# Kernel optimization log

Hardware: AMD Instinct MI355X
Metric: run time of the kernel (lower is better)

## Reference

```python
import jax, jax.numpy as jnp
import numpy as np

B, N, NNZ = 512, 512, 8192
ENTITY, EMB, HID = 30000, 64, 100
PAD_ID = ENTITY - 1


def setup_inputs() -> dict:
    key = jax.random.key(0)
    ks = jax.random.split(key, 8)
    hyperneigh = jax.random.randint(ks[0], (B, N), 0, PAD_ID, dtype=jnp.int64)
    adj_rows = jax.random.randint(ks[1], (B, NNZ), 0, N, dtype=jnp.int32)
    adj_cols = jax.random.randint(ks[2], (B, NNZ), 0, N, dtype=jnp.int32)
    adj_vals = jax.random.uniform(ks[3], (B, NNZ), dtype=jnp.float32)
    emb_table = jax.random.normal(ks[4], (ENTITY, EMB), dtype=jnp.float32)
    emb_table = emb_table.at[PAD_ID].set(0.0)  # padding_idx row is zero
    stdv1 = 1.0 / np.sqrt(HID)
    W1 = jax.random.uniform(ks[5], (EMB, HID), minval=-stdv1, maxval=stdv1, dtype=jnp.float32)
    b1 = jax.random.uniform(ks[6], (HID,), minval=-stdv1, maxval=stdv1, dtype=jnp.float32)
    k7, k8 = jax.random.split(ks[7])
    W2 = jax.random.uniform(k7, (HID, HID), minval=-stdv1, maxval=stdv1, dtype=jnp.float32)
    b2 = jax.random.uniform(k8, (HID,), minval=-stdv1, maxval=stdv1, dtype=jnp.float32)
    return dict(hyperneigh=hyperneigh, adj_rows=adj_rows, adj_cols=adj_cols,
                adj_vals=adj_vals, emb_table=emb_table, W1=W1, b1=b1, W2=W2, b2=b2)


def _spmm(rows, cols, vals, X):
    # sparse [N,N] @ X[N,H] via gather + segment_sum (COO, fixed nnz)
    msgs = vals[:, None] * X[cols]  # [nnz, H]
    return jax.ops.segment_sum(msgs, rows, num_segments=N)

_batched_spmm = jax.vmap(_spmm, in_axes=(0, 0, 0, 0))


def reference(hyperneigh, adj_rows, adj_cols, adj_vals, emb_table, W1, b1, W2, b2):
    # embedding lookup: [B, N, EMB]
    x = emb_table[hyperneigh]
    # HGNN_conv layer 1: support = X @ W; out = A @ support + bias
    support = jnp.einsum('bne,eh->bnh', x, W1)
    x = _batched_spmm(adj_rows, adj_cols, adj_vals, support) + b1
    # HGNN_conv layer 2
    support = jnp.einsum('bnh,hk->bnk', x, W2)
    x = _batched_spmm(adj_rows, adj_cols, adj_vals, support) + b2
    return x  # [B, N, HID]
```

## Files before the change

### kernel.cpp

```cpp
#include <hip/hip_runtime.h>

#define BB   512
#define NN   512
#define NNZ  8192
#define EMB  64
#define HID  100
#define EXCAP 128

#define OFF_RC      0
#define OFF_VPK     16777216
#define OFF_SSTART  25165824
#define OFF_SUPT    26216448
#define OFF_W1T     84936704
#define OFF_W2T     84951040

typedef __attribute__((ext_vector_type(8))) short short8;
typedef __attribute__((ext_vector_type(4))) float floatx4;

__device__ __forceinline__ unsigned short f2bf(float f) {
    unsigned u = __float_as_uint(f);
    unsigned r = (u + 0x7fffu + ((u >> 16) & 1u)) >> 16;
    return (unsigned short)r;
}

__device__ __forceinline__ float bf2f(unsigned short b) {
    return __uint_as_float((unsigned)b << 16);
}

__device__ __forceinline__ short8 pack8(float4 a, float4 b) {
    short8 s;
    s[0] = (short)f2bf(a.x); s[1] = (short)f2bf(a.y);
    s[2] = (short)f2bf(a.z); s[3] = (short)f2bf(a.w);
    s[4] = (short)f2bf(b.x); s[5] = (short)f2bf(b.y);
    s[6] = (short)f2bf(b.z); s[7] = (short)f2bf(b.w);
    return s;
}

__device__ __forceinline__ size_t supt_addr(int batch, int col, int k) {
    return (size_t)batch * 57344 + (size_t)(k >> 5) * 3584 + (size_t)col * 32 + (k & 31);
}

__device__ __forceinline__ int ad_addr(int rr, int c) {
    return (rr >> 4) * 8192 + (c >> 5) * 512 + ((c >> 3) & 3) * 128 + (rr & 15) * 8 + (c & 7);
}

__global__ __launch_bounds__(512) void k_bucket(
    const int* __restrict__ rows, const int* __restrict__ cols,
    const float* __restrict__ vals, int* __restrict__ rc,
    unsigned short* __restrict__ vpk, int* __restrict__ sstart,
    const float* __restrict__ W1, const float* __restrict__ W2,
    unsigned short* __restrict__ w1t, unsigned short* __restrict__ w2t)
{
    __shared__ int            rl[NNZ];
    __shared__ unsigned short vh[NNZ];
    __shared__ int            wcnt[8][8];
    __shared__ int            wbase[8][8];

    const int b   = blockIdx.x;
    const int tid = threadIdx.x;
    const int lane = tid & 63, wave = tid >> 6;

    {
        int pid = b + (tid << 9);
        if (pid < 7168) {
            int h = pid >> 6, k = pid & 63;
            w1t[pid] = f2bf((h < 100) ? W1[k * 100 + h] : 0.f);
        } else if (pid < 7168 + 14336) {
            int id2 = pid - 7168;
            int h = id2 >> 7, k = id2 & 127;
            w2t[id2] = f2bf((h < 100 && k < 100) ? W2[k * 100 + h] : 0.f);
        }
    }

    const int*   rb = rows + (size_t)b * NNZ;
    const int*   cb = cols + (size_t)b * NNZ;
    const float* vb = vals + (size_t)b * NNZ;

    int rr[16], cc[16];
    float vv[16];
    #pragma unroll
    for (int i = 0; i < 16; ++i) {
        int idx = tid + i * 512;
        rr[i] = rb[idx]; cc[i] = cb[idx]; vv[i] = vb[idx];
    }

    if (tid < 64) ((int*)wcnt)[tid] = 0;
    __syncthreads();

    #pragma unroll
    for (int i = 0; i < 16; ++i)
        atomicAdd(&wcnt[wave][rr[i] >> 6], 1);
    __syncthreads();

    if (tid == 0) {
        int acc = 0;
        #pragma unroll
        for (int s = 0; s < 8; ++s) {
            sstart[b * 9 + s] = acc;
            #pragma unroll
            for (int w = 0; w < 8; ++w) { wbase[w][s] = acc; acc += wcnt[w][s]; }
        }
        sstart[b * 9 + 8] = NNZ;
    }
    __syncthreads();
    if (tid < 64) ((int*)wcnt)[tid] = ((int*)wbase)[tid];
    __syncthreads();

    #pragma unroll
    for (int i = 0; i < 16; ++i) {
        int s = rr[i] >> 6;
        int pos = atomicAdd(&wcnt[wave][s], 1);
        rl[pos] = (rr[i] << 16) | cc[i];
        vh[pos] = f2bf(vv[i]);
    }
    __syncthreads();

    {
        int* orc = rc + (size_t)b * NNZ;
        #pragma unroll
        for (int i = 0; i < 16; ++i) {
            int idx = tid + i * 512;
            orc[idx] = rl[idx];
        }
        unsigned* ov = (unsigned*)(vpk + (size_t)b * NNZ);
        #pragma unroll
        for (int i = 0; i < 8; ++i) {
            int p = tid + i * 512;
            ov[p] = (unsigned)vh[2 * p] | ((unsigned)vh[2 * p + 1] << 16);
        }
    }
}

__global__ __launch_bounds__(256) void k_gemm1_mfma(
    const int* __restrict__ hyper, const float* __restrict__ emb,
    const unsigned short* __restrict__ w1t, unsigned short* __restrict__ supT)
{
    const int lane = threadIdx.x & 63, wave = threadIdx.x >> 6;
    const int l15 = lane & 15, g4 = lane >> 4;

    short8 bq[7][2];
    #pragma unroll
    for (int ct = 0; ct < 7; ++ct)
        #pragma unroll
        for (int kt = 0; kt < 2; ++kt)
            bq[ct][kt] = *(const short8*)(w1t + (ct * 16 + l15) * 64 + kt * 32 + g4 * 8);

    const int wsid = blockIdx.x * 4 + wave;
    #pragma unroll 2
    for (int i = 0; i < 4; ++i) {
        const int  rb   = wsid * 4 + i;
        const long base = (long)rb * 16;
        const int  rid  = hyper[base + l15];
        const float* ep = emb + (long)rid * EMB + g4 * 8;
        float4 f0 = *(const float4*)(ep);
        float4 f1 = *(const float4*)(ep + 4);
        float4 f2 = *(const float4*)(ep + 32);
        float4 f3 = *(const float4*)(ep + 36);
        short8 a0 = pack8(f0, f1);
        short8 a1 = pack8(f2, f3);

        floatx4 acc[7];
        #pragma unroll
        for (int ct = 0; ct < 7; ++ct) acc[ct] = (floatx4)0.f;
        #pragma unroll
        for (int ct = 0; ct < 7; ++ct) {
            acc[ct] = __builtin_amdgcn_mfma_f32_16x16x32_bf16(a0, bq[ct][0], acc[ct], 0, 0, 0);
            acc[ct] = __builtin_amdgcn_mfma_f32_16x16x32_bf16(a1, bq[ct][1], acc[ct], 0, 0, 0);
        }

        const int batch = rb >> 5;
        const int inrow = (rb & 31) * 16 + g4 * 4;
        #pragma unroll
        for (int ct = 0; ct < 7; ++ct) {
            int col = ct * 16 + l15;
            uint2 w;
            w.x = (unsigned)f2bf(acc[ct][0]) | ((unsigned)f2bf(acc[ct][1]) << 16);
            w.y = (unsigned)f2bf(acc[ct][2]) | ((unsigned)f2bf(acc[ct][3]) << 16);
            *(uint2*)(supT + supt_addr(batch, col, inrow)) = w;
        }
    }
}

__global__ __launch_bounds__(256) void k_gemm2_mfma(
    const unsigned short* __restrict__ h1, const unsigned short* __restrict__ w2t,
    unsigned short* __restrict__ supT)
{
    const int lane = threadIdx.x & 63, wave = threadIdx.x >> 6;
    const int l15 = lane & 15, g4 = lane >> 4;
    const int ct0 = (wave & 1) ? 4 : 0;

    short8 bq[4][4];
    #pragma unroll
    for (int ctl = 0; ctl < 4; ++ctl) {
        int ct = ct0 + ctl;
        if (ct < 7)
            #pragma unroll
            for (int kt = 0; kt < 4; ++kt)
                bq[ctl][kt] = *(const short8*)(w2t + (ct * 16 + l15) * 128 + kt * 32 + g4 * 8);
    }

    const int wp = blockIdx.x * 2 + (wave >> 1);
    #pragma unroll 2
    for (int i = 0; i < 8; ++i) {
        const int  rb   = wp * 8 + i;
        const long base = (long)rb * 16;
        const unsigned short* rp = h1 + (size_t)(base + l15) * 112;

        short8 a[4];
        #pragma unroll
        for (int kt = 0; kt < 4; ++kt) {
            int k0 = kt * 32 + g4 * 8;
            short8 av = (short8)(short)0;
            if (k0 < 112) av = *(const short8*)(rp + k0);
            a[kt] = av;
        }

        floatx4 acc[4];
        #pragma unroll
        for (int ctl = 0; ctl < 4; ++ctl) acc[ctl] = (floatx4)0.f;
        #pragma unroll
        for (int ctl = 0; ctl < 4; ++ctl) {
            if (ct0 + ctl < 7) {
                #pragma unroll
                for (int kt = 0; kt < 4; ++kt)
                    acc[ctl] = __builtin_amdgcn_mfma_f32_16x16x32_bf16(a[kt], bq[ctl][kt], acc[ctl], 0, 0, 0);
            }
        }

        const int batch = rb >> 5;
        const int inrow = (rb & 31) * 16 + g4 * 4;
        #pragma unroll
        for (int ctl = 0; ctl < 4; ++ctl) {
            if (ct0 + ctl < 7) {
                int col = (ct0 + ctl) * 16 + l15;
                uint2 w;
                w.x = (unsigned)f2bf(acc[ctl][0]) | ((unsigned)f2bf(acc[ctl][1]) << 16);
                w.y = (unsigned)f2bf(acc[ctl][2]) | ((unsigned)f2bf(acc[ctl][3]) << 16);
                *(uint2*)(supT + supt_addr(batch, col, inrow)) = w;
            }
        }
    }
}

template<bool FINAL>
__global__ __launch_bounds__(512, 4) void k_spmm_mfma(
    const int* __restrict__ sstart, const int* __restrict__ rc,
    const unsigned short* __restrict__ vpk, const unsigned short* __restrict__ supT,
    const float* __restrict__ bias, unsigned short* __restrict__ h1,
    float* __restrict__ out)
{
    __shared__ unsigned short Ad[64 * 512];
    __shared__ unsigned       bmap[64 * 16];
    __shared__ int            exc_rc[EXCAP];
    __shared__ unsigned short exc_v[EXCAP];
    __shared__ int            exn;

    const int tid    = threadIdx.x;
    const int xcd    = blockIdx.x & 7;
    const int local  = blockIdx.x >> 3;
    const int batch  = xcd * 64 + (local >> 3);
    const int stripe = local & 7;
    const int r0     = stripe * 64;

    const int lane = tid & 63, wave = tid >> 6;
    const int l15 = lane & 15, g4 = lane >> 4;
    const int ng  = wave & 3, kh = wave >> 2;
    const int nt0 = ng * 2;
    const bool two = (nt0 + 1) < 7;
    const int ktb = kh * 8;

    const int s0 = sstart[batch * 9 + stripe];
    const int e0 = sstart[batch * 9 + stripe + 1];
    const int*            rcb = rc + (size_t)batch * NNZ;
    const unsigned short* vvb = vpk + (size_t)batch * NNZ;
    int            pc[3];
    unsigned short pv[3];
    #pragma unroll
    for (int i = 0; i < 3; ++i) {
        int idx = s0 + tid + i * 512;
        bool ok = idx < e0;
        pc[i] = ok ? rcb[idx] : 0;
        pv[i] = ok ? vvb[idx] : 0;
    }

    const unsigned short* b0p = supT + (size_t)batch * 57344 + (size_t)ktb * 3584
                               + (nt0 * 16 + l15) * 32 + g4 * 8;
    const unsigned short* b1p = b0p + 512;
    short8 bfr[8];
    #pragma unroll
    for (int kt = 0; kt < 8; ++kt)
        bfr[kt] = *(const short8*)(b0p + (size_t)kt * 3584);

    {
        uint4* z = (uint4*)Ad;
        #pragma unroll
        for (int i = 0; i < 8; ++i) z[tid + i * 512] = make_uint4(0u, 0u, 0u, 0u);
        if (tid < 256) ((uint4*)bmap)[tid] = make_uint4(0u, 0u, 0u, 0u);
        if (tid == 0) exn = 0;
    }
    __syncthreads();

    #pragma unroll
    for (int i = 0; i < 3; ++i) {
        int idx = s0 + tid + i * 512;
        if (idx < e0) {
            int rr = ((pc[i] >> 16) & 0xffff) - r0;
            int c  = pc[i] & 0xffff;
            unsigned bit = 1u << (c & 31);
            unsigned old = atomicOr(&bmap[(rr << 4) + (c >> 5)], bit);
            if (old & bit) {
                int e = atomicAdd(&exn, 1);
                if (e < EXCAP) { exc_rc[e] = (rr << 9) | c; exc_v[e] = pv[i]; }
            } else {
                Ad[ad_addr(rr, c)] = pv[i];
            }
        }
    }
    for (int idx = s0 + 1536 + tid; idx < e0; idx += 512) {
        int p = rcb[idx];
        int rr = ((p >> 16) & 0xffff) - r0;
        int c  = p & 0xffff;
        unsigned bit = 1u << (c & 31);
        unsigned old = atomicOr(&bmap[(rr << 4) + (c >> 5)], bit);
        if (old & bit) {
            int e = atomicAdd(&exn, 1);
            if (e < EXCAP) { exc_rc[e] = (rr << 9) | c; exc_v[e] = vvb[idx]; }
        } else {
            Ad[ad_addr(rr, c)] = vvb[idx];
        }
    }
    __syncthreads();

    {
        int ne = exn < EXCAP ? exn : EXCAP;
        for (int t = tid; t < ne; t += 512) {
            int key = exc_rc[t];
            bool first = true;
            for (int j = 0; j < t; ++j)
                if (exc_rc[j] == key) { first = false; break; }
            if (first) {
                float add = bf2f(exc_v[t]);
                for (int j = t + 1; j < ne; ++j)
                    if (exc_rc[j] == key) add += bf2f(exc_v[j]);
                int rr = key >> 9, c = key & 511;
                int a = ad_addr(rr, c);
                Ad[a] = f2bf(bf2f(Ad[a]) + add);
            }
        }
    }
    __syncthreads();

    const unsigned short* ap = Ad + (size_t)ktb * 512 + lane * 8;

    floatx4 acc[2][4];
    #pragma unroll
    for (int n = 0; n < 2; ++n)
        #pragma unroll
        for (int m = 0; m < 4; ++m) acc[n][m] = (floatx4)0.f;

    #pragma unroll
    for (int kt = 0; kt < 8; ++kt) {
        short8 b1 = (short8)(short)0;
        if (two) b1 = *(const short8*)(b1p + (size_t)kt * 3584);
        #pragma unroll
        for (int m = 0; m < 4; ++m) {
            short8 a = *(const short8*)(ap + m * 8192 + kt * 512);
            acc[0][m] = __builtin_amdgcn_mfma_f32_16x16x32_bf16(a, bfr[kt], acc[0][m], 0, 0, 0);
            if (two)
                acc[1][m] = __builtin_amdgcn_mfma_f32_16x16x32_bf16(a, b1, acc[1][m], 0, 0, 0);
        }
    }
    __syncthreads();

    float* redu = (float*)Ad;
    if (kh == 1) {
        #pragma unroll
        for (int nn = 0; nn < 2; ++nn)
            #pragma unroll
            for (int m = 0; m < 4; ++m)
                #pragma unroll
                for (int q = 0; q < 4; ++q)
                    redu[ng * 2048 + ((nn * 4 + m) * 4 + q) * 64 + lane] = acc[nn][m][q];
    }
    __syncthreads();

    if (kh == 0) {
        #pragma unroll
        for (int nn = 0; nn < 2; ++nn)
            #pragma unroll
            for (int m = 0; m < 4; ++m)
                #pragma unroll
                for (int q = 0; q < 4; ++q)
                    acc[nn][m][q] += redu[ng * 2048 + ((nn * 4 + m) * 4 + q) * 64 + lane];

        if (FINAL) {
            float* st = (float*)((char*)Ad + 32768);
            #pragma unroll
            for (int nn = 0; nn < 2; ++nn) {
                int nt = nt0 + nn;
                if (nt >= 7) break;
                int col = nt * 16 + l15;
                float bi = (col < HID) ? bias[col] : 0.f;
                #pragma unroll
                for (int m = 0; m < 4; ++m) {
                    int row = m * 16 + g4 * 4;
                    #pragma unroll
                    for (int q = 0; q < 4; ++q)
                        st[(row + q) * 112 + col] = acc[nn][m][q] + bi;
                }
            }
        } else {
            unsigned short* st = (unsigned short*)((char*)Ad + 32768);
            #pragma unroll
            for (int nn = 0; nn < 2; ++nn) {
                int nt = nt0 + nn;
                if (nt >= 7) break;
                int col = nt * 16 + l15;
                float bi = (col < HID) ? bias[col] : 0.f;
                #pragma unroll
                for (int m = 0; m < 4; ++m) {
                    int row = m * 16 + g4 * 4;
                    #pragma unroll
                    for (int q = 0; q < 4; ++q)
                        st[(row + q) * 112 + col] = f2bf(acc[nn][m][q] + bi);
                }
            }
        }
    }
    __syncthreads();

    if (FINAL) {
        const float* st = (const float*)((char*)Ad + 32768);
        #pragma unroll
        for (int i = 0; i < 4; ++i) {
            int flat = tid + i * 512;
            if (flat < 1600) {
                int row = flat / 25, wi = flat - row * 25;
                float4 v = *(const float4*)(st + row * 112 + wi * 4);
                *(float4*)(out + ((size_t)batch * NN + r0 + row) * HID + wi * 4) = v;
            }
        }
    } else {
        const unsigned short* st = (const unsigned short*)((char*)Ad + 32768);
        #pragma unroll
        for (int i = 0; i < 2; ++i) {
            int flat = tid + i * 512;
            if (flat < 896) {
                int row = flat / 14, wi = flat - row * 14;
                uint4 v = *(const uint4*)(st + row * 112 + wi * 8);
                *(uint4*)(h1 + ((size_t)batch * NN + r0 + row) * 112 + wi * 8) = v;
            }
        }
    }
}

extern "C" void kernel_launch(void* const* d_in, const int* in_sizes, int n_in,
                              void* d_out, int out_size, void* d_ws, size_t ws_size,
                              hipStream_t stream)
{
    const int*   hyper = (const int*)  d_in[0];
    const int*   arows = (const int*)  d_in[1];
    const int*   acols = (const int*)  d_in[2];
    const float* avals = (const float*)d_in[3];
    const float* emb   = (const float*)d_in[4];
    const float* W1    = (const float*)d_in[5];
    const float* b1    = (const float*)d_in[6];
    const float* W2    = (const float*)d_in[7];
    const float* b2    = (const float*)d_in[8];

    float*          out = (float*)d_out;
    unsigned short* h1  = (unsigned short*)d_out;
    char*           ws  = (char*)d_ws;

    int*            rc     = (int*)           (ws + OFF_RC);
    unsigned short* vpk    = (unsigned short*)(ws + OFF_VPK);
    int*            sstart = (int*)           (ws + OFF_SSTART);
    unsigned short* supT   = (unsigned short*)(ws + OFF_SUPT);
    unsigned short* w1t    = (unsigned short*)(ws + OFF_W1T);
    unsigned short* w2t    = (unsigned short*)(ws + OFF_W2T);

    k_bucket<<<BB, 512, 0, stream>>>(arows, acols, avals, rc, vpk, sstart,
                                     W1, W2, w1t, w2t);

    k_gemm1_mfma<<<1024, 256, 0, stream>>>(hyper, emb, w1t, supT);
    k_spmm_mfma<false><<<BB * 8, 512, 0, stream>>>(sstart, rc, vpk, supT, b1, h1, out);
    k_gemm2_mfma<<<1024, 256, 0, stream>>>(h1, w2t, supT);
    k_spmm_mfma<true><<<BB * 8, 512, 0, stream>>>(sstart, rc, vpk, supT, b2, h1, out);
}
```

Before: 236.2 us.

## Detect duplicate COO entries once in bucket kernel instead of per spmm

Duplicate (row,col) detection moves from each spmm launch into the bucketing kernel. It uses a global bitmap (memset each call) and a per-batch exception list, with duplicates marked by a sentinel column. Each spmm then scatters non-duplicates into the dense tile without shared atomics and adds the exceptions from a preloaded list. The B-fragment loads also move into the MFMA loop with partial unroll, which lowers register use. The cost is a 16MB global memset plus global atomics in the bucket kernel, and every stripe block scans the whole batch's exception list.

```diff
diff --git a/kernel.cpp b/kernel.cpp
--- a/kernel.cpp
+++ b/kernel.cpp
@@ -5,7 +5,8 @@
 #define NNZ  8192
 #define EMB  64
 #define HID  100
-#define EXCAP 128
+#define EXCAPB 512
+#define DUPC 0x7FFF
 
 #define OFF_RC      0
 #define OFF_VPK     16777216
@@ -13,6 +14,10 @@
 #define OFF_SUPT    26216448
 #define OFF_W1T     84936704
 #define OFF_W2T     84951040
+#define OFF_BMAPG   84979712
+#define OFF_EXCNT   101756928
+#define OFF_EXK     101758976
+#define OFF_EXV     102807552
 
 typedef __attribute__((ext_vector_type(8))) short short8;
 typedef __attribute__((ext_vector_type(4))) float floatx4;
@@ -48,6 +53,8 @@
     const int* __restrict__ rows, const int* __restrict__ cols,
     const float* __restrict__ vals, int* __restrict__ rc,
     unsigned short* __restrict__ vpk, int* __restrict__ sstart,
+    unsigned* __restrict__ bmap_g, int* __restrict__ exc_cnt,
+    int* __restrict__ exc_k, float* __restrict__ exc_v,
     const float* __restrict__ W1, const float* __restrict__ W2,
     unsigned short* __restrict__ w1t, unsigned short* __restrict__ w2t)
 {
@@ -58,7 +65,7 @@
 
     const int b   = blockIdx.x;
     const int tid = threadIdx.x;
-    const int lane = tid & 63, wave = tid >> 6;
+    const int wave = tid >> 6;
 
     {
         int pid = b + (tid << 9);
@@ -84,6 +91,24 @@
         rr[i] = rb[idx]; cc[i] = cb[idx]; vv[i] = vb[idx];
     }
 
+    unsigned* bm = bmap_g + (size_t)b * 8192;
+    unsigned dupmask = 0;
+    #pragma unroll
+    for (int i = 0; i < 16; ++i) {
+        unsigned bit = 1u << (cc[i] & 31);
+        unsigned old = atomicOr(&bm[(rr[i] << 4) + (cc[i] >> 5)], bit);
+        if (old & bit) {
+            dupmask |= 1u << i;
+            int e = atomicAdd(&exc_cnt[b], 1);
+            if (e < EXCAPB) {
+                exc_k[b * EXCAPB + e] = (rr[i] << 9) | cc[i];
+                exc_v[b * EXCAPB + e] = vv[i];
+            } else {
+                dupmask &= ~(1u << i);
+            }
+        }
+    }
+
     if (tid < 64) ((int*)wcnt)[tid] = 0;
     __syncthreads();
 
@@ -110,8 +135,9 @@
     for (int i = 0; i < 16; ++i) {
         int s = rr[i] >> 6;
         int pos = atomicAdd(&wcnt[wave][s], 1);
-        rl[pos] = (rr[i] << 16) | cc[i];
-        vh[pos] = f2bf(vv[i]);
+        bool dup = (dupmask >> i) & 1;
+        rl[pos] = (rr[i] << 16) | (dup ? DUPC : cc[i]);
+        vh[pos] = dup ? 0 : f2bf(vv[i]);
     }
     __syncthreads();
 
@@ -246,14 +272,13 @@
 __global__ __launch_bounds__(512, 4) void k_spmm_mfma(
     const int* __restrict__ sstart, const int* __restrict__ rc,
     const unsigned short* __restrict__ vpk, const unsigned short* __restrict__ supT,
-    const float* __restrict__ bias, unsigned short* __restrict__ h1,
-    float* __restrict__ out)
+    const int* __restrict__ exc_cnt, const int* __restrict__ exc_k,
+    const float* __restrict__ exc_v, const float* __restrict__ bias,
+    unsigned short* __restrict__ h1, float* __restrict__ out)
 {
     __shared__ unsigned short Ad[64 * 512];
-    __shared__ unsigned       bmap[64 * 16];
-    __shared__ int            exc_rc[EXCAP];
-    __shared__ unsigned short exc_v[EXCAP];
-    __shared__ int            exn;
+    __shared__ int            lk[EXCAPB];
+    __shared__ float          lv[EXCAPB];
 
     const int tid    = threadIdx.x;
     const int xcd    = blockIdx.x & 7;
@@ -271,6 +296,7 @@
 
     const int s0 = sstart[batch * 9 + stripe];
     const int e0 = sstart[batch * 9 + stripe + 1];
+    const int ne = min(exc_cnt[batch], EXCAPB);
     const int*            rcb = rc + (size_t)batch * NNZ;
     const unsigned short* vvb = vpk + (size_t)batch * NNZ;
     int            pc[3];
@@ -282,21 +308,15 @@
         pc[i] = ok ? rcb[idx] : 0;
         pv[i] = ok ? vvb[idx] : 0;
     }
-
-    const unsigned short* b0p = supT + (size_t)batch * 57344 + (size_t)ktb * 3584
-                               + (nt0 * 16 + l15) * 32 + g4 * 8;
-    const unsigned short* b1p = b0p + 512;
-    short8 bfr[8];
-    #pragma unroll
-    for (int kt = 0; kt < 8; ++kt)
-        bfr[kt] = *(const short8*)(b0p + (size_t)kt * 3584);
+    if (tid < ne) {
+        lk[tid] = exc_k[batch * EXCAPB + tid];
+        lv[tid] = exc_v[batch * EXCAPB + tid];
+    }
 
     {
         uint4* z = (uint4*)Ad;
         #pragma unroll
         for (int i = 0; i < 8; ++i) z[tid + i * 512] = make_uint4(0u, 0u, 0u, 0u);
-        if (tid < 256) ((uint4*)bmap)[tid] = make_uint4(0u, 0u, 0u, 0u);
-        if (tid == 0) exn = 0;
     }
     __syncthreads();
 
@@ -306,51 +326,39 @@
         if (idx < e0) {
             int rr = ((pc[i] >> 16) & 0xffff) - r0;
             int c  = pc[i] & 0xffff;
-            unsigned bit = 1u << (c & 31);
-            unsigned old = atomicOr(&bmap[(rr << 4) + (c >> 5)], bit);
-            if (old & bit) {
-                int e = atomicAdd(&exn, 1);
-                if (e < EXCAP) { exc_rc[e] = (rr << 9) | c; exc_v[e] = pv[i]; }
-            } else {
-                Ad[ad_addr(rr, c)] = pv[i];
-            }
+            if (c < 512) Ad[ad_addr(rr, c)] = pv[i];
         }
     }
     for (int idx = s0 + 1536 + tid; idx < e0; idx += 512) {
         int p = rcb[idx];
         int rr = ((p >> 16) & 0xffff) - r0;
         int c  = p & 0xffff;
-        unsigned bit = 1u << (c & 31);
-        unsigned old = atomicOr(&bmap[(rr << 4) + (c >> 5)], bit);
-        if (old & bit) {
-            int e = atomicAdd(&exn, 1);
-            if (e < EXCAP) { exc_rc[e] = (rr << 9) | c; exc_v[e] = vvb[idx]; }
-        } else {
-            Ad[ad_addr(rr, c)] = vvb[idx];
-        }
-    }
-    __syncthreads();
-
-    {
-        int ne = exn < EXCAP ? exn : EXCAP;
-        for (int t = tid; t < ne; t += 512) {
-            int key = exc_rc[t];
-            bool first = true;
-            for (int j = 0; j < t; ++j)
-                if (exc_rc[j] == key) { first = false; break; }
-            if (first) {
-                float add = bf2f(exc_v[t]);
-                for (int j = t + 1; j < ne; ++j)
-                    if (exc_rc[j] == key) add += bf2f(exc_v[j]);
-                int rr = key >> 9, c = key & 511;
-                int a = ad_addr(rr, c);
-                Ad[a] = f2bf(bf2f(Ad[a]) + add);
-            }
-        }
-    }
-    __syncthreads();
-
-    const unsigned short* ap = Ad + (size_t)ktb * 512 + lane * 8;
+        if (c < 512) Ad[ad_addr(rr, c)] = vvb[idx];
+    }
+    __syncthreads();
+
+    for (int t = tid; t < ne; t += 512) {
+        int key = lk[t];
+        int r   = key >> 9;
+        if ((r >> 6) != stripe) continue;
+        bool first = true;
+        for (int j = 0; j < t; ++j)
+            if (lk[j] == key) { first = false; break; }
+        if (first) {
+            float add = lv[t];
+            for (int j = t + 1; j < ne; ++j)
+                if (lk[j] == key) add += lv[j];
+            int rr = r & 63, c = key & 511;
+            int a = ad_addr(rr, c);
+            Ad[a] = f2bf(bf2f(Ad[a]) + add);
+        }
+    }
+    __syncthreads();
+
+    const unsigned short* b0p = supT + (size_t)batch * 57344 + (size_t)ktb * 3584
+                               + (nt0 * 16 + l15) * 32 + g4 * 8;
+    const unsigned short* b1p = b0p + 512;
+    const unsigned short* ap  = Ad + (size_t)ktb * 512 + lane * 8;
 
     floatx4 acc[2][4];
     #pragma unroll
@@ -358,14 +366,15 @@
         #pragma unroll
         for (int m = 0; m < 4; ++m) acc[n][m] = (floatx4)0.f;
 
-    #pragma unroll
+    #pragma unroll 4
     for (int kt = 0; kt < 8; ++kt) {
+        short8 b0 = *(const short8*)(b0p + (size_t)kt * 3584);
         short8 b1 = (short8)(short)0;
         if (two) b1 = *(const short8*)(b1p + (size_t)kt * 3584);
         #pragma unroll
         for (int m = 0; m < 4; ++m) {
             short8 a = *(const short8*)(ap + m * 8192 + kt * 512);
-            acc[0][m] = __builtin_amdgcn_mfma_f32_16x16x32_bf16(a, bfr[kt], acc[0][m], 0, 0, 0);
+            acc[0][m] = __builtin_amdgcn_mfma_f32_16x16x32_bf16(a, b0, acc[0][m], 0, 0, 0);
             if (two)
                 acc[1][m] = __builtin_amdgcn_mfma_f32_16x16x32_bf16(a, b1, acc[1][m], 0, 0, 0);
         }
@@ -478,12 +487,20 @@
     unsigned short* supT   = (unsigned short*)(ws + OFF_SUPT);
     unsigned short* w1t    = (unsigned short*)(ws + OFF_W1T);
     unsigned short* w2t    = (unsigned short*)(ws + OFF_W2T);
+    unsigned*       bmapg  = (unsigned*)      (ws + OFF_BMAPG);
+    int*            excnt  = (int*)           (ws + OFF_EXCNT);
+    int*            exck   = (int*)           (ws + OFF_EXK);
+    float*          excv   = (float*)         (ws + OFF_EXV);
+
+    hipMemsetAsync(bmapg, 0, 16777216 + 2048, stream);
 
     k_bucket<<<BB, 512, 0, stream>>>(arows, acols, avals, rc, vpk, sstart,
-                                     W1, W2, w1t, w2t);
+                                     bmapg, excnt, exck, excv, W1, W2, w1t, w2t);
 
     k_gemm1_mfma<<<1024, 256, 0, stream>>>(hyper, emb, w1t, supT);
-    k_spmm_mfma<false><<<BB * 8, 512, 0, stream>>>(sstart, rc, vpk, supT, b1, h1, out);
+    k_spmm_mfma<false><<<BB * 8, 512, 0, stream>>>(sstart, rc, vpk, supT,
+                                                   excnt, exck, excv, b1, h1, out);
     k_gemm2_mfma<<<1024, 256, 0, stream>>>(h1, w2t, supT);
-    k_spmm_mfma<true><<<BB * 8, 512, 0, stream>>>(sstart, rc, vpk, supT, b2, h1, out);
-}
+    k_spmm_mfma<true><<<BB * 8, 512, 0, stream>>>(sstart, rc, vpk, supT,
+                                                  excnt, exck, excv, b2, h1, out);
+}
```

Result: slower. 622.0 us (+163.3%).

## Resolve duplicate COO entries once in bucketing kernel instead of per spmm

Applied to the files above, without the earlier changes.

Duplicate (row,col) detection and merging moves from the two spmm kernels into the one-time bucketing kernel. Duplicates are marked with a sentinel column and their values are folded into the first occurrence, so the spmm kernels drop the bitmap atomics, exception list and serial merge pass. The spmm kernel also preloads both B fragments into registers before the MFMA loop. The cost is more LDS and a linear search per duplicate group in the bucketing kernel, plus higher register pressure in spmm.

```diff
diff --git a/kernel.cpp b/kernel.cpp
--- a/kernel.cpp
+++ b/kernel.cpp
@@ -5,7 +5,8 @@
 #define NNZ  8192
 #define EMB  64
 #define HID  100
-#define EXCAP 128
+#define EXC  384
+#define DUPC 0x7FFF
 
 #define OFF_RC      0
 #define OFF_VPK     16777216
@@ -51,14 +52,19 @@
     const float* __restrict__ W1, const float* __restrict__ W2,
     unsigned short* __restrict__ w1t, unsigned short* __restrict__ w2t)
 {
-    __shared__ int            rl[NNZ];
-    __shared__ unsigned short vh[NNZ];
-    __shared__ int            wcnt[8][8];
-    __shared__ int            wbase[8][8];
-
-    const int b   = blockIdx.x;
-    const int tid = threadIdx.x;
-    const int lane = tid & 63, wave = tid >> 6;
+    __shared__ int      rl[NNZ];
+    __shared__ unsigned ub[NN * 16];
+    __shared__ int      wcnt[8][8];
+    __shared__ int      wbase[8][8];
+    __shared__ int      exk[EXC];
+    __shared__ float    exv[EXC];
+    __shared__ int      exn;
+
+    unsigned short* vh = (unsigned short*)ub;
+
+    const int b    = blockIdx.x;
+    const int tid  = threadIdx.x;
+    const int wave = tid >> 6;
 
     {
         int pid = b + (tid << 9);
@@ -84,12 +90,27 @@
         rr[i] = rb[idx]; cc[i] = cb[idx]; vv[i] = vb[idx];
     }
 
+    #pragma unroll
+    for (int i = 0; i < 16; ++i) ub[tid + i * 512] = 0u;
     if (tid < 64) ((int*)wcnt)[tid] = 0;
-    __syncthreads();
-
-    #pragma unroll
-    for (int i = 0; i < 16; ++i)
+    if (tid == 0) exn = 0;
+    __syncthreads();
+
+    unsigned dupmask = 0;
+    #pragma unroll
+    for (int i = 0; i < 16; ++i) {
+        unsigned bit = 1u << (cc[i] & 31);
+        unsigned old = atomicOr(&ub[(rr[i] << 4) + (cc[i] >> 5)], bit);
+        if (old & bit) {
+            int e = atomicAdd(&exn, 1);
+            if (e < EXC) {
+                dupmask |= 1u << i;
+                exk[e] = (rr[i] << 16) | cc[i];
+                exv[e] = vv[i];
+            }
+        }
         atomicAdd(&wcnt[wave][rr[i] >> 6], 1);
+    }
     __syncthreads();
 
     if (tid == 0) {
@@ -110,8 +131,34 @@
     for (int i = 0; i < 16; ++i) {
         int s = rr[i] >> 6;
         int pos = atomicAdd(&wcnt[wave][s], 1);
-        rl[pos] = (rr[i] << 16) | cc[i];
-        vh[pos] = f2bf(vv[i]);
+        bool dup = (dupmask >> i) & 1;
+        rl[pos] = (rr[i] << 16) | (dup ? DUPC : cc[i]);
+        vh[pos] = dup ? 0 : f2bf(vv[i]);
+    }
+    __syncthreads();
+
+    {
+        int ne = exn < EXC ? exn : EXC;
+        for (int t = tid; t < ne; t += 512) {
+            int key = exk[t];
+            bool first = true;
+            for (int j = 0; j < t; ++j)
+                if (exk[j] == key) { first = false; break; }
+            if (first) {
+                float add = exv[t];
+                for (int j = t + 1; j < ne; ++j)
+                    if (exk[j] == key) add += exv[j];
+                int s  = (key >> 16) >> 6;
+                int lo = wbase[0][s];
+                int hi = (s < 7) ? wbase[0][s + 1] : NNZ;
+                for (int j = lo; j < hi; ++j) {
+                    if (rl[j] == key) {
+                        vh[j] = f2bf(bf2f(vh[j]) + add);
+                        break;
+                    }
+                }
+            }
+        }
     }
     __syncthreads();
 
@@ -250,10 +297,6 @@
     float* __restrict__ out)
 {
     __shared__ unsigned short Ad[64 * 512];
-    __shared__ unsigned       bmap[64 * 16];
-    __shared__ int            exc_rc[EXCAP];
-    __shared__ unsigned short exc_v[EXCAP];
-    __shared__ int            exn;
 
     const int tid    = threadIdx.x;
     const int xcd    = blockIdx.x & 7;
@@ -286,17 +329,18 @@
     const unsigned short* b0p = supT + (size_t)batch * 57344 + (size_t)ktb * 3584
                                + (nt0 * 16 + l15) * 32 + g4 * 8;
     const unsigned short* b1p = b0p + 512;
-    short8 bfr[8];
-    #pragma unroll
-    for (int kt = 0; kt < 8; ++kt)
-        bfr[kt] = *(const short8*)(b0p + (size_t)kt * 3584);
+    short8 bfr[16];
+    #pragma unroll
+    for (int kt = 0; kt < 8; ++kt) {
+        bfr[2 * kt] = *(const short8*)(b0p + (size_t)kt * 3584);
+        if (two) bfr[2 * kt + 1] = *(const short8*)(b1p + (size_t)kt * 3584);
+        else     bfr[2 * kt + 1] = (short8)(short)0;
+    }
 
     {
         uint4* z = (uint4*)Ad;
         #pragma unroll
         for (int i = 0; i < 8; ++i) z[tid + i * 512] = make_uint4(0u, 0u, 0u, 0u);
-        if (tid < 256) ((uint4*)bmap)[tid] = make_uint4(0u, 0u, 0u, 0u);
-        if (tid == 0) exn = 0;
     }
     __syncthreads();
 
@@ -306,47 +350,14 @@
         if (idx < e0) {
             int rr = ((pc[i] >> 16) & 0xffff) - r0;
             int c  = pc[i] & 0xffff;
-            unsigned bit = 1u << (c & 31);
-            unsigned old = atomicOr(&bmap[(rr << 4) + (c >> 5)], bit);
-            if (old & bit) {
-                int e = atomicAdd(&exn, 1);
-                if (e < EXCAP) { exc_rc[e] = (rr << 9) | c; exc_v[e] = pv[i]; }
-            } else {
-                Ad[ad_addr(rr, c)] = pv[i];
-            }
+            if (c < 512) Ad[ad_addr(rr, c)] = pv[i];
         }
     }
     for (int idx = s0 + 1536 + tid; idx < e0; idx += 512) {
         int p = rcb[idx];
         int rr = ((p >> 16) & 0xffff) - r0;
         int c  = p & 0xffff;
-        unsigned bit = 1u << (c & 31);
-        unsigned old = atomicOr(&bmap[(rr << 4) + (c >> 5)], bit);
-        if (old & bit) {
-            int e = atomicAdd(&exn, 1);
-            if (e < EXCAP) { exc_rc[e] = (rr << 9) | c; exc_v[e] = vvb[idx]; }
-        } else {
-            Ad[ad_addr(rr, c)] = vvb[idx];
-        }
-    }
-    __syncthreads();
-
-    {
-        int ne = exn < EXCAP ? exn : EXCAP;
-        for (int t = tid; t < ne; t += 512) {
-            int key = exc_rc[t];
-            bool first = true;
-            for (int j = 0; j < t; ++j)
-                if (exc_rc[j] == key) { first = false; break; }
-            if (first) {
-                float add = bf2f(exc_v[t]);
-                for (int j = t + 1; j < ne; ++j)
-                    if (exc_rc[j] == key) add += bf2f(exc_v[j]);
-                int rr = key >> 9, c = key & 511;
-                int a = ad_addr(rr, c);
-                Ad[a] = f2bf(bf2f(Ad[a]) + add);
-            }
-        }
+        if (c < 512) Ad[ad_addr(rr, c)] = vvb[idx];
     }
     __syncthreads();
 
@@ -360,14 +371,12 @@
 
     #pragma unroll
     for (int kt = 0; kt < 8; ++kt) {
-        short8 b1 = (short8)(short)0;
-        if (two) b1 = *(const short8*)(b1p + (size_t)kt * 3584);
         #pragma unroll
         for (int m = 0; m < 4; ++m) {
             short8 a = *(const short8*)(ap + m * 8192 + kt * 512);
-            acc[0][m] = __builtin_amdgcn_mfma_f32_16x16x32_bf16(a, bfr[kt], acc[0][m], 0, 0, 0);
+            acc[0][m] = __builtin_amdgcn_mfma_f32_16x16x32_bf16(a, bfr[2 * kt], acc[0][m], 0, 0, 0);
             if (two)
-                acc[1][m] = __builtin_amdgcn_mfma_f32_16x16x32_bf16(a, b1, acc[1][m], 0, 0, 0);
+                acc[1][m] = __builtin_amdgcn_mfma_f32_16x16x32_bf16(a, bfr[2 * kt + 1], acc[1][m], 0, 0, 0);
         }
     }
     __syncthreads();
```

Measured after the change: 296.5 us. 25.5% more time.
